# Kernel optimization log

Hardware: AMD Instinct MI355X
Metric: run time of the kernel (lower is better)

The kernel has to match this reference:

```python
import jax, jax.numpy as jnp
import numpy as np

B, T = 4, 2048
N_EMBD = 1024
TIME_EMBD = 128
N_HEAD = 16
C_IN = N_EMBD + TIME_EMBD  # 1152


def setup_inputs() -> dict:
    key = jax.random.key(0)
    ks = jax.random.split(key, 7)
    s_in = 1.0 / np.sqrt(C_IN)
    s_e = 1.0 / np.sqrt(N_EMBD)
    return {
        "x": jax.random.normal(ks[0], (B, T, C_IN), jnp.float32),
        "ln_w": jnp.ones((C_IN,), jnp.float32),
        "ln_b": jnp.zeros((C_IN,), jnp.float32),
        "W_attn": jax.random.normal(ks[1], (C_IN, 3 * N_EMBD), jnp.float32) * s_in,
        "b_attn": jax.random.normal(ks[2], (3 * N_EMBD,), jnp.float32) * 0.01,
        "W_proj": jax.random.normal(ks[3], (N_EMBD, N_EMBD), jnp.float32) * s_e,
        "b_proj": jax.random.normal(ks[4], (N_EMBD,), jnp.float32) * 0.01,
    }


def _layernorm(x, w, b, eps=1e-5):
    mu = jnp.mean(x, axis=-1, keepdims=True)
    var = jnp.var(x, axis=-1, keepdims=True)
    return (x - mu) * jax.lax.rsqrt(var + eps) * w + b


def reference(x, ln_w, ln_b, W_attn, b_attn, W_proj, b_proj):
    h = _layernorm(x, ln_w, ln_b)                      # [B,T,C_IN]
    qkv = h @ W_attn + b_attn                          # [B,T,3*N_EMBD]
    q, k, v = jnp.split(qkv, 3, axis=-1)
    hd = N_EMBD // N_HEAD
    q = q.reshape(B, T, N_HEAD, hd).transpose(0, 2, 1, 3)  # [B,H,T,hd]
    k = k.reshape(B, T, N_HEAD, hd).transpose(0, 2, 1, 3)
    v = v.reshape(B, T, N_HEAD, hd).transpose(0, 2, 1, 3)
    att = jnp.einsum("bhqd,bhkd->bhqk", q, k) * (1.0 / np.sqrt(hd))
    mask = jnp.tril(jnp.ones((T, T), bool))
    att = jnp.where(mask, att, -jnp.inf)
    att = jax.nn.softmax(att, axis=-1)                 # dropout p=0 -> identity
    y = jnp.einsum("bhqk,bhkd->bhqd", att, v)          # [B,H,T,hd]
    y = y.transpose(0, 2, 1, 3).reshape(B, T, N_EMBD)
    return y @ W_proj + b_proj
```

## Files before the change

kernel.cpp:

```cpp
#include <hip/hip_runtime.h>
#include <hip/hip_bf16.h>

#define BB 4
#define TT 2048
#define C_IN 1152
#define NE 1024
#define NH 16
#define HD 64
#define MM (BB*TT)
#define N_QKV (3*NE)

typedef __attribute__((ext_vector_type(8))) short s16x8;
typedef __attribute__((ext_vector_type(4))) float f32x4;

static __device__ __forceinline__ unsigned short f2bf(float x) {
    unsigned int u = __float_as_uint(x);
    unsigned int r = (u + 0x7fffu + ((u >> 16) & 1u)) >> 16;
    return (unsigned short)r;
}

static __device__ __forceinline__ void async16(const void* g, void* l) {
    __builtin_amdgcn_global_load_lds((const __attribute__((address_space(1))) void*)g,
                                     (__attribute__((address_space(3))) void*)l, 16, 0, 0);
}

__global__ __launch_bounds__(256) void ln_kernel(const float* __restrict__ x,
                                                 const float* __restrict__ w,
                                                 const float* __restrict__ b,
                                                 unsigned short* __restrict__ h) {
    const int row = blockIdx.x;
    const float* xr = x + (size_t)row * C_IN;
    float s = 0.f, sq = 0.f;
    for (int i = threadIdx.x; i < C_IN; i += 256) {
        float v = xr[i];
        s += v; sq += v * v;
    }
    for (int off = 1; off < 64; off <<= 1) {
        s  += __shfl_xor(s, off, 64);
        sq += __shfl_xor(sq, off, 64);
    }
    __shared__ float red[2][4];
    const int wid = threadIdx.x >> 6, lane = threadIdx.x & 63;
    if (lane == 0) { red[0][wid] = s; red[1][wid] = sq; }
    __syncthreads();
    s  = red[0][0] + red[0][1] + red[0][2] + red[0][3];
    sq = red[1][0] + red[1][1] + red[1][2] + red[1][3];
    const float mu  = s * (1.f / C_IN);
    const float var = sq * (1.f / C_IN) - mu * mu;
    const float rs  = rsqrtf(var + 1e-5f);
    unsigned short* hr = h + (size_t)row * C_IN;
    for (int i = threadIdx.x; i < C_IN; i += 256) {
        float v = (xr[i] - mu) * rs * w[i] + b[i];
        hr[i] = f2bf(v);
    }
}

__global__ __launch_bounds__(256) void transpose_cast(const float* __restrict__ in,
                                                      unsigned short* __restrict__ out,
                                                      int K, int N) {
    __shared__ float tile[32][33];
    const int n0 = blockIdx.x * 32, k0 = blockIdx.y * 32;
    const int tx = threadIdx.x & 31, ty = threadIdx.x >> 5;
    for (int i = ty; i < 32; i += 8)
        tile[i][tx] = in[(size_t)(k0 + i) * N + n0 + tx];
    __syncthreads();
    for (int i = ty; i < 32; i += 8)
        out[(size_t)(n0 + i) * K + k0 + tx] = f2bf(tile[tx][i]);
}

#define ATT_SC 0.18033688011112042f

#define EP_STRIDE 136
template <int MODE>
__global__ __launch_bounds__(256) void gemm_bt(const unsigned short* __restrict__ A,
                                               const unsigned short* __restrict__ Bt,
                                               const float* __restrict__ bias,
                                               void* __restrict__ outp,
                                               unsigned short* __restrict__ kb,
                                               unsigned short* __restrict__ vt,
                                               int M, int N, int K) {
    __shared__ unsigned short smem[32768];
    const int tid = threadIdx.x;
    const int wid = tid >> 6, lane = tid & 63;
    const int wm = wid >> 1, wn = wid & 1;
    const int quad = lane >> 4, l16 = lane & 15;

    const int gx  = gridDim.x;
    const int nwg = gx * gridDim.y;
    const int bid = blockIdx.y * gx + blockIdx.x;
    const int wg  = (bid & 7) * (nwg >> 3) + (bid >> 3);
    const int m0 = (wg / gx) * 128, n0 = (wg % gx) * 128;

    const int rl = lane >> 3;
    const int sc = (lane & 7) ^ rl;
    const unsigned short* gA = A  + (size_t)(m0 + wid * 32 + rl) * K + sc * 8;
    const unsigned short* gB = Bt + (size_t)(n0 + wid * 32 + rl) * K + sc * 8;

    f32x4 acc[4][4] = {};
    const int nk = K >> 6;

    const int sc0 = (quad ^ (l16 & 7)) * 8;
    const int sc1 = ((4 + quad) ^ (l16 & 7)) * 8;

#define STAGE(KT, BUF)                                                          \
    {                                                                           \
        const unsigned short* a_ = gA + (KT) * 64;                              \
        const unsigned short* b_ = gB + (KT) * 64;                              \
        unsigned short* sa_ = &smem[(BUF) * 16384 + wid * 2048];                \
        unsigned short* sb_ = &smem[(BUF) * 16384 + 8192 + wid * 2048];         \
        _Pragma("unroll")                                                       \
        for (int j = 0; j < 4; j++) {                                           \
            async16(a_ + (size_t)(j * 8) * K, sa_ + j * 512);                   \
            async16(b_ + (size_t)(j * 8) * K, sb_ + j * 512);                   \
        }                                                                       \
    }

    STAGE(0, 0);

    for (int kt = 0; kt < nk; kt++) {
        __syncthreads();
        const int cur = kt & 1;
        if (kt + 1 < nk) STAGE(kt + 1, cur ^ 1);

        const unsigned short* As_ = &smem[cur * 16384];
        const unsigned short* Bs_ = &smem[cur * 16384 + 8192];
        #pragma unroll
        for (int h = 0; h < 2; h++) {
            const int sch = h ? sc1 : sc0;
            s16x8 af[4], bfb[4];
            #pragma unroll
            for (int mi = 0; mi < 4; mi++)
                af[mi] = *(const s16x8*)&As_[(wm * 64 + mi * 16 + l16) * 64 + sch];
            #pragma unroll
            for (int ni = 0; ni < 4; ni++)
                bfb[ni] = *(const s16x8*)&Bs_[(wn * 64 + ni * 16 + l16) * 64 + sch];
            #pragma unroll
            for (int mi = 0; mi < 4; mi++)
                #pragma unroll
                for (int ni = 0; ni < 4; ni++)
                    acc[mi][ni] = __builtin_amdgcn_mfma_f32_16x16x32_bf16(af[mi], bfb[ni], acc[mi][ni], 0, 0, 0);
        }
    }
#undef STAGE

    const int which0 = n0 >> 10;
    const float sc_ = (MODE == 0 && which0 == 0) ? ATT_SC : 1.0f;
    for (int ni = 0; ni < 4; ni++) {
        const float bv = bias[n0 + wn * 64 + ni * 16 + l16];
        for (int mi = 0; mi < 4; mi++)
            for (int r = 0; r < 4; r++)
                acc[mi][ni][r] = (acc[mi][ni][r] + bv) * sc_;
    }

    if (MODE == 1) {
        float* Tf = (float*)smem;
        float* out = (float*)outp;
        for (int p = 0; p < 2; p++) {
            __syncthreads();
            if (wm == p) {
                for (int mi = 0; mi < 4; mi++)
                    for (int ni = 0; ni < 4; ni++) {
                        const int col = wn * 64 + ni * 16 + l16;
                        for (int r = 0; r < 4; r++)
                            Tf[(mi * 16 + quad * 4 + r) * 128 + col] = acc[mi][ni][r];
                    }
            }
            __syncthreads();
            const int rlo = tid >> 5;
            const int c4 = (tid & 31) * 4;
            for (int rr = rlo; rr < 64; rr += 8) {
                *(float4*)&out[(size_t)(m0 + p * 64 + rr) * N + n0 + c4] =
                    *(const float4*)&Tf[rr * 128 + c4];
            }
        }
        return;
    }

    const int which = n0 >> 10;
    const int bb = m0 >> 11;
    const int mloc = m0 & 2047;
    unsigned short* T = smem;

    if (which < 2) {
        unsigned short* qk = (which == 0) ? (unsigned short*)outp : kb;
        for (int pass = 0; pass < 2; pass++) {
            __syncthreads();
            if (wm == pass) {
                for (int mi = 0; mi < 4; mi++)
                    for (int ni = 0; ni < 4; ni++) {
                        const int nl = wn * 64 + ni * 16 + l16;
                        for (int r = 0; r < 4; r++)
                            T[(mi * 16 + quad * 4 + r) * EP_STRIDE + nl] = f2bf(acc[mi][ni][r]);
                    }
            }
            __syncthreads();
            const int ml = tid >> 2, c = tid & 3;
            const int t  = mloc + pass * 64 + ml;
            const int nl0 = c * 32;
            const int hh = ((n0 & 1023) >> 6) + (nl0 >> 6);
            const int d0 = nl0 & 63;
            unsigned short* dst = qk + ((size_t)(bb * 16 + hh) * TT + t) * HD + d0;
            const unsigned short* src = &T[ml * EP_STRIDE + nl0];
            for (int u = 0; u < 4; u++)
                *(s16x8*)(dst + u * 8) = *(const s16x8*)(src + u * 8);
        }
    } else {
        for (int pass = 0; pass < 2; pass++) {
            __syncthreads();
            if (wn == pass) {
                for (int mi = 0; mi < 4; mi++)
                    for (int ni = 0; ni < 4; ni++) {
                        const int nlh = ni * 16 + l16;
                        const int mlb = wm * 64 + mi * 16 + quad * 4;
                        for (int r = 0; r < 4; r += 2) {
                            const unsigned int pk = (unsigned int)f2bf(acc[mi][ni][r]) |
                                                    ((unsigned int)f2bf(acc[mi][ni][r + 1]) << 16);
                            *(unsigned int*)&T[nlh * EP_STRIDE + mlb + r] = pk;
                        }
                    }
            }
            __syncthreads();
            const int nlh = tid >> 2, c = tid & 3;
            const int hh = (n0 - 2048 + pass * 64) >> 6;
            unsigned short* dst = vt + ((size_t)(bb * 16 + hh) * HD + nlh) * TT + mloc + c * 32;
            const unsigned short* src = &T[nlh * EP_STRIDE + c * 32];
            for (int u = 0; u < 4; u++)
                *(s16x8*)(dst + u * 8) = *(const s16x8*)(src + u * 8);
        }
    }
}

#define PST 72

__global__ __launch_bounds__(256) void attn_kernel(const unsigned short* __restrict__ qb,
                                                   const unsigned short* __restrict__ kb,
                                                   const unsigned short* __restrict__ vt,
                                                   unsigned short* __restrict__ yb) {
    __shared__ unsigned short Ks[2][64 * 64];
    __shared__ unsigned short Vs[2][64 * 64];
    __shared__ unsigned short Ps[4][2 * 16 * PST];
    const int tid = threadIdx.x, wid = tid >> 6, lane = tid & 63;
    const int quad = lane >> 4, l16 = lane & 15;
    const int bh = blockIdx.x & 63;
    const int qblk = 15 - (blockIdx.x >> 6);

    const unsigned short* qh = qb + (size_t)bh * TT * HD;
    const unsigned short* kh = kb + (size_t)bh * TT * HD;
    const unsigned short* vh = vt + (size_t)bh * HD * TT;
    unsigned short* ps = Ps[wid];

    const int q0w = qblk * 128 + wid * 32;
    s16x8 aq[2][2];
    #pragma unroll
    for (int mf = 0; mf < 2; mf++) {
        aq[mf][0] = *(const s16x8*)&qh[(size_t)(q0w + mf * 16 + l16) * HD + quad * 8];
        aq[mf][1] = *(const s16x8*)&qh[(size_t)(q0w + mf * 16 + l16) * HD + 32 + quad * 8];
    }
    s16x8 onesf;
    #pragma unroll
    for (int i = 0; i < 8; i++) onesf[i] = (short)0x3F80;

    f32x4 yacc[2][4] = {};
    f32x4 lacc[2] = {};
    const int ntiles = 2 * qblk + 2;

    const int rl = lane >> 3;
    const int cc = (lane & 7) ^ (rl & 7);
    const unsigned short* kp0 = kh + (size_t)(wid * 16 + rl) * HD + cc * 8;
    const unsigned short* kp1 = kh + (size_t)(wid * 16 + 8 + rl) * HD + cc * 8;
    const unsigned short* vp0 = vh + (size_t)(wid * 16 + rl) * TT + cc * 8;
    const unsigned short* vp1 = vh + (size_t)(wid * 16 + 8 + rl) * TT + cc * 8;
    const int ldsK0 = wid * 16 * 64, ldsK1 = (wid * 16 + 8) * 64;

    async16(kp0, &Ks[0][ldsK0]);  async16(kp1, &Ks[0][ldsK1]);
    async16(vp0, &Vs[0][ldsK0]);  async16(vp1, &Vs[0][ldsK1]);
    kp0 += 64 * HD; kp1 += 64 * HD; vp0 += 64; vp1 += 64;

    const int p0s = quad ^ (l16 & 7);
    const int p1s = (4 + quad) ^ (l16 & 7);

#define ATT_STEP(CUR, TT_)                                                              \
    {                                                                                   \
        __syncthreads();                                                                \
        if ((TT_) + 1 < ntiles) {                                                       \
            async16(kp0, &Ks[(CUR) ^ 1][ldsK0]);  async16(kp1, &Ks[(CUR) ^ 1][ldsK1]);  \
            async16(vp0, &Vs[(CUR) ^ 1][ldsK0]);  async16(vp1, &Vs[(CUR) ^ 1][ldsK1]);  \
            kp0 += 64 * HD; kp1 += 64 * HD; vp0 += 64; vp1 += 64;                       \
        }                                                                               \
        const int tk0 = (TT_) * 64;                                                     \
        if (tk0 <= q0w + 31) {                                                          \
            const unsigned short* Kc = Ks[CUR];                                         \
            const unsigned short* Vc = Vs[CUR];                                         \
            s16x8 kf[4][2], vf[4][2];                                                   \
            _Pragma("unroll")                                                           \
            for (int nj = 0; nj < 4; nj++) {                                            \
                kf[nj][0] = *(const s16x8*)&Kc[(nj * 16 + l16) * 64 + p0s * 8];         \
                kf[nj][1] = *(const s16x8*)&Kc[(nj * 16 + l16) * 64 + p1s * 8];         \
            }                                                                           \
            _Pragma("unroll")                                                           \
            for (int ni = 0; ni < 4; ni++) {                                            \
                vf[ni][0] = *(const s16x8*)&Vc[(ni * 16 + l16) * 64 + p0s * 8];         \
                vf[ni][1] = *(const s16x8*)&Vc[(ni * 16 + l16) * 64 + p1s * 8];         \
            }                                                                           \
            _Pragma("unroll")                                                           \
            for (int mf = 0; mf < 2; mf++) {                                            \
                const int f0 = q0w + mf * 16;                                           \
                if (tk0 > f0 + 15) continue;                                            \
                unsigned short* pm = ps + mf * (16 * PST);                              \
                const int qg = f0 + l16;                                                \
                f32x4 st[4];                                                            \
                _Pragma("unroll")                                                       \
                for (int nj = 0; nj < 4; nj++) {                                        \
                    f32x4 z = {};                                                       \
                    z = __builtin_amdgcn_mfma_f32_16x16x32_bf16(kf[nj][0], aq[mf][0], z, 0, 0, 0); \
                    z = __builtin_amdgcn_mfma_f32_16x16x32_bf16(kf[nj][1], aq[mf][1], z, 0, 0, 0); \
                    st[nj] = z;                                                         \
                }                                                                       \
                const bool diag = (tk0 + 64 > f0);                                      \
                float pv[4][4];                                                         \
                _Pragma("unroll")                                                       \
                for (int nj = 0; nj < 4; nj++)                                          \
                    _Pragma("unroll")                                                   \
                    for (int r = 0; r < 4; r++)                                         \
                        pv[nj][r] = exp2f(st[nj][r]);                                   \
                if (diag) {                                                             \
                    _Pragma("unroll")                                                   \
                    for (int nj = 0; nj < 4; nj++) {                                    \
                        const int keyb = tk0 + nj * 16 + quad * 4;                      \
                        _Pragma("unroll")                                               \
                        for (int r = 0; r < 4; r++)                                     \
                            if (keyb + r > qg) pv[nj][r] = 0.f;                         \
                    }                                                                   \
                }                                                                       \
                _Pragma("unroll")                                                       \
                for (int nj = 0; nj < 4; nj++) {                                        \
                    const unsigned int pk0 = __builtin_amdgcn_perm(                     \
                        __float_as_uint(pv[nj][1]), __float_as_uint(pv[nj][0]), 0x07060302u); \
                    const unsigned int pk1 = __builtin_amdgcn_perm(                     \
                        __float_as_uint(pv[nj][3]), __float_as_uint(pv[nj][2]), 0x07060302u); \
                    *(uint2*)&pm[l16 * PST + nj * 16 + quad * 4] = make_uint2(pk0, pk1);\
                }                                                                       \
                __asm volatile("s_waitcnt lgkmcnt(0)" ::: "memory");                    \
                const s16x8 ap0 = *(const s16x8*)&pm[l16 * PST + quad * 8];             \
                const s16x8 ap1 = *(const s16x8*)&pm[l16 * PST + 32 + quad * 8];        \
                lacc[mf] = __builtin_amdgcn_mfma_f32_16x16x32_bf16(ap0, onesf, lacc[mf], 0, 0, 0); \
                lacc[mf] = __builtin_amdgcn_mfma_f32_16x16x32_bf16(ap1, onesf, lacc[mf], 0, 0, 0); \
                _Pragma("unroll")                                                       \
                for (int ni = 0; ni < 4; ni++) {                                        \
                    yacc[mf][ni] = __builtin_amdgcn_mfma_f32_16x16x32_bf16(ap0, vf[ni][0], yacc[mf][ni], 0, 0, 0); \
                    yacc[mf][ni] = __builtin_amdgcn_mfma_f32_16x16x32_bf16(ap1, vf[ni][1], yacc[mf][ni], 0, 0, 0); \
                }                                                                       \
            }                                                                           \
        }                                                                               \
    }

    for (int t = 0; t < ntiles; t += 2) {
        ATT_STEP(0, t);
        ATT_STEP(1, t + 1);
    }
#undef ATT_STEP

    const int bbi = bh >> 4, hh = bh & 15;
    #pragma unroll
    for (int mf = 0; mf < 2; mf++) {
        float linv[4];
        #pragma unroll
        for (int r = 0; r < 4; r++)
            linv[r] = 1.0f / lacc[mf][r];
        #pragma unroll
        for (int ni = 0; ni < 4; ni++)
            #pragma unroll
            for (int r = 0; r < 4; r++) {
                const int trow = q0w + mf * 16 + quad * 4 + r;
                yb[((size_t)bbi * TT + trow) * NE + hh * HD + ni * 16 + l16] =
                    f2bf(yacc[mf][ni][r] * linv[r]);
            }
    }
}

extern "C" void kernel_launch(void* const* d_in, const int* in_sizes, int n_in,
                              void* d_out, int out_size, void* d_ws, size_t ws_size,
                              hipStream_t stream) {
    const float* x      = (const float*)d_in[0];
    const float* ln_w   = (const float*)d_in[1];
    const float* ln_b   = (const float*)d_in[2];
    const float* W_attn = (const float*)d_in[3];
    const float* b_attn = (const float*)d_in[4];
    const float* W_proj = (const float*)d_in[5];
    const float* b_proj = (const float*)d_in[6];
    float* out = (float*)d_out;

    char* ws = (char*)d_ws;
    unsigned short* h    = (unsigned short*)ws;  ws += (size_t)MM * C_IN * 2;
    unsigned short* Wat  = (unsigned short*)ws;  ws += (size_t)N_QKV * C_IN * 2;
    unsigned short* Wpt  = (unsigned short*)ws;  ws += (size_t)NE * NE * 2;
    unsigned short* qbuf = (unsigned short*)ws;  ws += (size_t)MM * NE * 2;
    unsigned short* kbuf = (unsigned short*)ws;  ws += (size_t)MM * NE * 2;
    unsigned short* vtbf = (unsigned short*)ws;  ws += (size_t)MM * NE * 2;
    unsigned short* ybuf = (unsigned short*)ws;  ws += (size_t)MM * NE * 2;

    ln_kernel<<<MM, 256, 0, stream>>>(x, ln_w, ln_b, h);
    transpose_cast<<<dim3(N_QKV / 32, C_IN / 32), 256, 0, stream>>>(W_attn, Wat, C_IN, N_QKV);
    transpose_cast<<<dim3(NE / 32, NE / 32), 256, 0, stream>>>(W_proj, Wpt, NE, NE);
    gemm_bt<0><<<dim3(N_QKV / 128, MM / 128), 256, 0, stream>>>(h, Wat, b_attn, qbuf, kbuf, vtbf,
                                                                MM, N_QKV, C_IN);
    attn_kernel<<<64 * 16, 256, 0, stream>>>(qbuf, kbuf, vtbf, ybuf);
    gemm_bt<1><<<dim3(NE / 128, MM / 128), 256, 0, stream>>>(ybuf, Wpt, b_proj, out, nullptr, nullptr,
                                                             MM, NE, NE);
}
```

Measured before the change: 299.3 us.

## Vectorize layernorm, remap QKV GEMM tiles per XCD, single-pass epilogue, MFMA priority

Layernorm now loads each row once as float4 registers and reuses them for normalization, writing 4-wide bf16 stores, which removes the second global read of x. The QKV GEMM uses a new block-to-tile mapping that groups M/N tiles per XCD to improve L2 reuse of A and B. The QKV epilogue writes the whole 128x128 tile to LDS in one pass instead of two, cutting barriers. The attention kernel raises wave priority around the PV MFMA block. The mapping hardcodes the grid shape (96 tiles per group), so it breaks for other sizes.

Result: faster. 288.6 us (-3.6%).

```diff
diff --git a/kernel.cpp b/kernel.cpp
--- a/kernel.cpp
+++ b/kernel.cpp
@@ -11,6 +11,7 @@
 #define N_QKV (3*NE)
 
 typedef __attribute__((ext_vector_type(8))) short s16x8;
+typedef __attribute__((ext_vector_type(4))) short s16x4;
 typedef __attribute__((ext_vector_type(4))) float f32x4;
 
 static __device__ __forceinline__ unsigned short f2bf(float x) {
@@ -29,18 +30,20 @@
                                                  const float* __restrict__ b,
                                                  unsigned short* __restrict__ h) {
     const int row = blockIdx.x;
-    const float* xr = x + (size_t)row * C_IN;
-    float s = 0.f, sq = 0.f;
-    for (int i = threadIdx.x; i < C_IN; i += 256) {
-        float v = xr[i];
-        s += v; sq += v * v;
-    }
+    const int tid = threadIdx.x;
+    const float4* xr = (const float4*)(x + (size_t)row * C_IN);
+    const float4 a0 = xr[tid];
+    float4 a1 = make_float4(0.f, 0.f, 0.f, 0.f);
+    if (tid < 32) a1 = xr[256 + tid];
+    float s  = a0.x + a0.y + a0.z + a0.w + a1.x + a1.y + a1.z + a1.w;
+    float sq = a0.x*a0.x + a0.y*a0.y + a0.z*a0.z + a0.w*a0.w
+             + a1.x*a1.x + a1.y*a1.y + a1.z*a1.z + a1.w*a1.w;
     for (int off = 1; off < 64; off <<= 1) {
         s  += __shfl_xor(s, off, 64);
         sq += __shfl_xor(sq, off, 64);
     }
     __shared__ float red[2][4];
-    const int wid = threadIdx.x >> 6, lane = threadIdx.x & 63;
+    const int wid = tid >> 6, lane = tid & 63;
     if (lane == 0) { red[0][wid] = s; red[1][wid] = sq; }
     __syncthreads();
     s  = red[0][0] + red[0][1] + red[0][2] + red[0][3];
@@ -48,10 +51,26 @@
     const float mu  = s * (1.f / C_IN);
     const float var = sq * (1.f / C_IN) - mu * mu;
     const float rs  = rsqrtf(var + 1e-5f);
+    const float4* w4 = (const float4*)w;
+    const float4* b4 = (const float4*)b;
     unsigned short* hr = h + (size_t)row * C_IN;
-    for (int i = threadIdx.x; i < C_IN; i += 256) {
-        float v = (xr[i] - mu) * rs * w[i] + b[i];
-        hr[i] = f2bf(v);
+    {
+        const float4 wv = w4[tid], bv = b4[tid];
+        s16x4 o;
+        o[0] = (short)f2bf((a0.x - mu) * rs * wv.x + bv.x);
+        o[1] = (short)f2bf((a0.y - mu) * rs * wv.y + bv.y);
+        o[2] = (short)f2bf((a0.z - mu) * rs * wv.z + bv.z);
+        o[3] = (short)f2bf((a0.w - mu) * rs * wv.w + bv.w);
+        *(s16x4*)(hr + tid * 4) = o;
+    }
+    if (tid < 32) {
+        const float4 wv = w4[256 + tid], bv = b4[256 + tid];
+        s16x4 o;
+        o[0] = (short)f2bf((a1.x - mu) * rs * wv.x + bv.x);
+        o[1] = (short)f2bf((a1.y - mu) * rs * wv.y + bv.y);
+        o[2] = (short)f2bf((a1.z - mu) * rs * wv.z + bv.z);
+        o[3] = (short)f2bf((a1.w - mu) * rs * wv.w + bv.w);
+        *(s16x4*)(hr + (256 + tid) * 4) = o;
     }
 }
 
@@ -85,11 +104,24 @@
     const int wm = wid >> 1, wn = wid & 1;
     const int quad = lane >> 4, l16 = lane & 15;
 
-    const int gx  = gridDim.x;
-    const int nwg = gx * gridDim.y;
-    const int bid = blockIdx.y * gx + blockIdx.x;
-    const int wg  = (bid & 7) * (nwg >> 3) + (bid >> 3);
-    const int m0 = (wg / gx) * 128, n0 = (wg % gx) * 128;
+    int m0, n0;
+    if (MODE == 0) {
+        const int bid = blockIdx.y * gridDim.x + blockIdx.x;
+        const int xcd = bid & 7;
+        const int k   = bid >> 3;
+        const int mg  = k / 96;
+        const int r1  = k % 96;
+        const int ng  = r1 / 32;
+        const int rr  = r1 % 32;
+        m0 = (xcd * 8 + mg * 4 + (rr & 3)) * 128;
+        n0 = (ng * 8 + (rr >> 2)) * 128;
+    } else {
+        const int gx  = gridDim.x;
+        const int nwg = gx * gridDim.y;
+        const int bid = blockIdx.y * gx + blockIdx.x;
+        const int wg  = (bid & 7) * (nwg >> 3) + (bid >> 3);
+        m0 = (wg / gx) * 128; n0 = (wg % gx) * 128;
+    }
 
     const int rl = lane >> 3;
     const int sc = (lane & 7) ^ rl;
@@ -168,9 +200,9 @@
             __syncthreads();
             const int rlo = tid >> 5;
             const int c4 = (tid & 31) * 4;
-            for (int rr = rlo; rr < 64; rr += 8) {
-                *(float4*)&out[(size_t)(m0 + p * 64 + rr) * N + n0 + c4] =
-                    *(const float4*)&Tf[rr * 128 + c4];
+            for (int rr2 = rlo; rr2 < 64; rr2 += 8) {
+                *(float4*)&out[(size_t)(m0 + p * 64 + rr2) * N + n0 + c4] =
+                    *(const float4*)&Tf[rr2 * 128 + c4];
             }
         }
         return;
@@ -181,49 +213,49 @@
     const int mloc = m0 & 2047;
     unsigned short* T = smem;
 
+    __syncthreads();
+    if (which < 2) {
+        for (int mi = 0; mi < 4; mi++)
+            for (int ni = 0; ni < 4; ni++) {
+                const int nl = wn * 64 + ni * 16 + l16;
+                for (int r = 0; r < 4; r++)
+                    T[(wm * 64 + mi * 16 + quad * 4 + r) * EP_STRIDE + nl] = f2bf(acc[mi][ni][r]);
+            }
+    } else {
+        for (int mi = 0; mi < 4; mi++)
+            for (int ni = 0; ni < 4; ni++) {
+                const int nlh = wn * 64 + ni * 16 + l16;
+                const int mlb = wm * 64 + mi * 16 + quad * 4;
+                for (int r = 0; r < 4; r += 2) {
+                    const unsigned int pk = (unsigned int)f2bf(acc[mi][ni][r]) |
+                                            ((unsigned int)f2bf(acc[mi][ni][r + 1]) << 16);
+                    *(unsigned int*)&T[nlh * EP_STRIDE + mlb + r] = pk;
+                }
+            }
+    }
+    __syncthreads();
+
     if (which < 2) {
         unsigned short* qk = (which == 0) ? (unsigned short*)outp : kb;
-        for (int pass = 0; pass < 2; pass++) {
-            __syncthreads();
-            if (wm == pass) {
-                for (int mi = 0; mi < 4; mi++)
-                    for (int ni = 0; ni < 4; ni++) {
-                        const int nl = wn * 64 + ni * 16 + l16;
-                        for (int r = 0; r < 4; r++)
-                            T[(mi * 16 + quad * 4 + r) * EP_STRIDE + nl] = f2bf(acc[mi][ni][r]);
-                    }
-            }
-            __syncthreads();
-            const int ml = tid >> 2, c = tid & 3;
-            const int t  = mloc + pass * 64 + ml;
-            const int nl0 = c * 32;
-            const int hh = ((n0 & 1023) >> 6) + (nl0 >> 6);
-            const int d0 = nl0 & 63;
+        const int ml = tid >> 2, c = tid & 3;
+        const int nl0 = c * 32;
+        const int hh = ((n0 & 1023) >> 6) + (nl0 >> 6);
+        const int d0 = nl0 & 63;
+        for (int half = 0; half < 2; half++) {
+            const int row = half * 64 + ml;
+            const int t = mloc + row;
             unsigned short* dst = qk + ((size_t)(bb * 16 + hh) * TT + t) * HD + d0;
-            const unsigned short* src = &T[ml * EP_STRIDE + nl0];
+            const unsigned short* src = &T[row * EP_STRIDE + nl0];
             for (int u = 0; u < 4; u++)
                 *(s16x8*)(dst + u * 8) = *(const s16x8*)(src + u * 8);
         }
     } else {
-        for (int pass = 0; pass < 2; pass++) {
-            __syncthreads();
-            if (wn == pass) {
-                for (int mi = 0; mi < 4; mi++)
-                    for (int ni = 0; ni < 4; ni++) {
-                        const int nlh = ni * 16 + l16;
-                        const int mlb = wm * 64 + mi * 16 + quad * 4;
-                        for (int r = 0; r < 4; r += 2) {
-                            const unsigned int pk = (unsigned int)f2bf(acc[mi][ni][r]) |
-                                                    ((unsigned int)f2bf(acc[mi][ni][r + 1]) << 16);
-                            *(unsigned int*)&T[nlh * EP_STRIDE + mlb + r] = pk;
-                        }
-                    }
-            }
-            __syncthreads();
-            const int nlh = tid >> 2, c = tid & 3;
-            const int hh = (n0 - 2048 + pass * 64) >> 6;
-            unsigned short* dst = vt + ((size_t)(bb * 16 + hh) * HD + nlh) * TT + mloc + c * 32;
-            const unsigned short* src = &T[nlh * EP_STRIDE + c * 32];
+        const int nlh = tid >> 2, c = tid & 3;
+        const int hb = (n0 - 2048) >> 6;
+        for (int half = 0; half < 2; half++) {
+            const int row = half * 64 + nlh;
+            unsigned short* dst = vt + ((size_t)(bb * 16 + hb + half) * HD + nlh) * TT + mloc + c * 32;
+            const unsigned short* src = &T[row * EP_STRIDE + c * 32];
             for (int u = 0; u < 4; u++)
                 *(s16x8*)(dst + u * 8) = *(const s16x8*)(src + u * 8);
         }
@@ -341,6 +373,7 @@
                     *(uint2*)&pm[l16 * PST + nj * 16 + quad * 4] = make_uint2(pk0, pk1);\
                 }                                                                       \
                 __asm volatile("s_waitcnt lgkmcnt(0)" ::: "memory");                    \
+                __builtin_amdgcn_s_setprio(1);                                          \
                 const s16x8 ap0 = *(const s16x8*)&pm[l16 * PST + quad * 8];             \
                 const s16x8 ap1 = *(const s16x8*)&pm[l16 * PST + 32 + quad * 8];        \
                 lacc[mf] = __builtin_amdgcn_mfma_f32_16x16x32_bf16(ap0, onesf, lacc[mf], 0, 0, 0); \
@@ -350,6 +383,7 @@
                     yacc[mf][ni] = __builtin_amdgcn_mfma_f32_16x16x32_bf16(ap0, vf[ni][0], yacc[mf][ni], 0, 0, 0); \
                     yacc[mf][ni] = __builtin_amdgcn_mfma_f32_16x16x32_bf16(ap1, vf[ni][1], yacc[mf][ni], 0, 0, 0); \
                 }                                                                       \
+                __builtin_amdgcn_s_setprio(0);                                          \
             }                                                                           \
         }                                                                               \
     }
```
